# Kernel optimization log

Measured on AMD Instinct MI355X. Metric: run time of the kernel, lower is better.

The kernel has to match this reference:

```python
import jax, jax.numpy as jnp
import numpy as np


def setup_inputs() -> dict:
    key = jax.random.key(0)
    ks = jax.random.split(key, 8)
    B, D, H, W = 4, 96, 64, 64
    K, N, R = 4, 16, 6
    return {
        "x": jax.random.normal(ks[0], (B, D, H, W), jnp.float32),
        "x_proj_weight": jax.random.normal(ks[1], (K, R + 2 * N, D), jnp.float32) * 0.05,
        "dt_projs_weight": jax.random.normal(ks[2], (K, D, R), jnp.float32) * 0.1,
        "dt_projs_bias": jax.random.normal(ks[3], (K, D), jnp.float32) * 0.1,
        "A_logs": jax.random.uniform(ks[4], (K * D, N), jnp.float32),
        "Ds": jax.random.normal(ks[5], (K * D,), jnp.float32),
        "ln_weight": jnp.ones((D,), jnp.float32),
        "ln_bias": jnp.zeros((D,), jnp.float32),
    }


def reference(x, x_proj_weight, dt_projs_weight, dt_projs_bias, A_logs, Ds, ln_weight, ln_bias):
    B, D, H, W = x.shape
    K, _, R = dt_projs_weight.shape
    N = A_logs.shape[1]
    L = H * W

    # ---- CrossScan: 4 traversal orders (row-major, col-major, and their reverses) ----
    xf = x.reshape(B, D, L)                                   # row-major
    xt = jnp.transpose(x, (0, 1, 3, 2)).reshape(B, D, L)      # col-major
    xs = jnp.stack([xf, xt, xf[..., ::-1], xt[..., ::-1]], axis=1)  # (B, K, D, L)

    # ---- input-dependent projections ----
    x_dbl = jnp.einsum('bkdl,kcd->bkcl', xs, x_proj_weight)   # (B, K, R+2N, L)
    dts, Bs, Cs = jnp.split(x_dbl, [R, R + N], axis=2)        # Bs/Cs: (B, K, N, L)
    dts = jnp.einsum('bkrl,kdr->bkdl', dts, dt_projs_weight)  # (B, K, D, L)

    A = -jnp.exp(A_logs).reshape(K, D, N)                     # (K, D, N)
    delta = jax.nn.softplus(dts + dt_projs_bias[None, :, :, None])  # (B, K, D, L)

    # ---- selective (S6) scan over L ----
    def step(h, inp):
        d_t, u_t, B_t, C_t = inp  # (B,K,D) (B,K,D) (B,K,N) (B,K,N)
        dA = jnp.exp(d_t[..., None] * A[None])                # (B,K,D,N)
        h = h * dA + (d_t * u_t)[..., None] * B_t[:, :, None, :]
        y_t = jnp.einsum('bkdn,bkn->bkd', h, C_t)
        return h, y_t

    h0 = jnp.zeros((B, K, D, N), x.dtype)
    seq = (jnp.moveaxis(delta, -1, 0), jnp.moveaxis(xs, -1, 0),
           jnp.moveaxis(Bs, -1, 0), jnp.moveaxis(Cs, -1, 0))
    _, ys = jax.lax.scan(step, h0, seq)                       # (L, B, K, D)
    ys = jnp.moveaxis(ys, 0, -1)                              # (B, K, D, L)
    ys = ys + Ds.reshape(K, D)[None, :, :, None] * xs         # skip term D*u

    # ---- CrossMerge: undo the 4 traversal orders and sum ----
    m = ys[:, 0:2] + ys[:, 2:4][..., ::-1]                    # (B, 2, D, L)
    y = m[:, 0] + jnp.transpose(m[:, 1].reshape(B, D, W, H), (0, 1, 3, 2)).reshape(B, D, L)

    # ---- out_norm (LayerNorm over channels, v0 path) ----
    y = jnp.transpose(y, (0, 2, 1))                           # (B, L, D)
    mu = y.mean(-1, keepdims=True)
    var = y.var(-1, keepdims=True)
    y = (y - mu) / jnp.sqrt(var + 1e-5) * ln_weight + ln_bias
    return y.reshape(B, H, W, D)
```

## Files before the change

kernel.cpp:

```cpp
#include <hip/hip_runtime.h>
#include <math.h>

#define B_ 4
#define D_ 96
#define H_ 64
#define W_ 64
#define L_ 4096
#define K_ 4
#define N_ 16
#define R_ 6
#define C_ 38
#define SSX 128
#define CLSX (L_ / SSX)
#define CH_ (B_ * K_ * D_ * N_)

#if defined(__has_builtin)
#if __has_builtin(__builtin_amdgcn_exp2f)
#define EXP2F(x) __builtin_amdgcn_exp2f(x)
#else
#define EXP2F(x) exp2f(x)
#endif
#else
#define EXP2F(x) exp2f(x)
#endif
#define LOG2E 1.44269504f

__device__ __forceinline__ int src_idx(int k, int l) {
    int m = (k >= 2) ? (L_ - 1 - l) : l;
    if (k & 1) return ((m & 63) << 6) | (m >> 6);
    return m;
}

__device__ __forceinline__ float softplus_f(float a) {
    return (a > 15.f) ? a : __logf(1.f + __expf(a));
}

__global__ __launch_bounds__(256) void transpose_kernel(
    const float* __restrict__ x,
    float* __restrict__ xs2)
{
    int bid = blockIdx.x;
    int b = bid / (3 * 64);
    int rest = bid % (3 * 64);
    int dblk = rest / 64, lblk = rest % 64;
    int d0 = dblk * 32;
    int l0 = lblk * 64;
    int tid = threadIdx.x;

    __shared__ float s_t[32][65];

    for (int i = tid; i < 32 * 64; i += 256) {
        int d = i >> 6, l = i & 63;
        s_t[d][l] = x[((long)b * D_ + d0 + d) * L_ + l0 + l];
    }
    __syncthreads();

    for (int i = tid; i < 64 * 32; i += 256) {
        int l = i >> 5, d = i & 31;
        float v = s_t[d][l];
        xs2[((long)b * L_ + l0 + l) * D_ + d0 + d] = v;
        xs2[((long)(B_ + b) * L_ + l * 64 + lblk) * D_ + d0 + d] = v;
    }
}

__global__ __launch_bounds__(256) void proj_scan_kernel(
    const float* __restrict__ xs2,
    const float* __restrict__ xpw,
    const float* __restrict__ wdt,
    const float* __restrict__ bdt,
    const float* __restrict__ A_logs,
    float* __restrict__ delta,
    float* __restrict__ Bsb,
    float* __restrict__ Csb,
    float* __restrict__ pAarr,
    float* __restrict__ hharr)
{
    const int TL = 64;
    const int tiles = L_ / TL;
    int bid = blockIdx.x;
    int bk = bid / tiles;
    int tile = bid % tiles;
    int b = bk / K_, k = bk % K_;
    int l0 = tile * TL;
    int tid = threadIdx.x;

    __shared__ __align__(16) float s_wpT[D_ * 40];
    __shared__ __align__(16) float s_xs[D_ * 68];
    __shared__ __align__(16) float s_wdt[R_ * D_];
    __shared__ __align__(16) float s_bias[D_];
    __shared__ __align__(16) float s_dts[R_ * 68];
    __shared__ __align__(16) float s_B[TL * N_];

    for (int i = tid; i < C_ * D_; i += 256) {
        int d = i / C_, c = i % C_;
        int cp = (c < 6) ? c : c + 2;
        s_wpT[d * 40 + cp] = xpw[(k * C_ + c) * D_ + d];
    }
    for (int i = tid; i < 96; i += 256) {
        s_wpT[i * 40 + 6] = 0.f;
        s_wpT[i * 40 + 7] = 0.f;
    }
    for (int i = tid; i < R_ * D_; i += 256) {
        int r = i / D_, d = i % D_;
        s_wdt[i] = wdt[(k * D_ + d) * R_ + r];
    }
    if (tid < D_) s_bias[tid] = bdt[k * D_ + tid];

    const float* xsp = xs2 + (long)((k & 1) * B_ + b) * L_ * D_;
    for (int i = tid; i < TL * 24; i += 256) {
        int lt = i / 24, dq = i % 24;
        int row = (k < 2) ? (l0 + lt) : (L_ - 1 - l0 - lt);
        float4 v = *(const float4*)(xsp + (long)row * D_ + dq * 4);
        s_xs[(dq * 4 + 0) * 68 + lt] = v.x;
        s_xs[(dq * 4 + 1) * 68 + lt] = v.y;
        s_xs[(dq * 4 + 2) * 68 + lt] = v.z;
        s_xs[(dq * 4 + 3) * 68 + lt] = v.w;
    }
    __syncthreads();

    long base = (long)bk * L_ + l0;

    int ct = tid >> 4;
    int lt4 = (tid & 15) * 4;
    if (ct < 10) {
        int cp0 = ct * 4;
        float acc[4][4];
#pragma unroll
        for (int i = 0; i < 4; ++i)
#pragma unroll
            for (int j = 0; j < 4; ++j) acc[i][j] = 0.f;
#pragma unroll 4
        for (int d = 0; d < D_; ++d) {
            float4 wv = *(const float4*)(&s_wpT[d * 40 + cp0]);
            float4 xv = *(const float4*)(&s_xs[d * 68 + lt4]);
            float wa[4] = {wv.x, wv.y, wv.z, wv.w};
            float xa[4] = {xv.x, xv.y, xv.z, xv.w};
#pragma unroll
            for (int ci = 0; ci < 4; ++ci)
#pragma unroll
                for (int li = 0; li < 4; ++li)
                    acc[ci][li] += wa[ci] * xa[li];
        }
        if (ct == 0) {
#pragma unroll
            for (int ci = 0; ci < 4; ++ci)
                *(float4*)(&s_dts[ci * 68 + lt4]) =
                    make_float4(acc[ci][0], acc[ci][1], acc[ci][2], acc[ci][3]);
        } else if (ct == 1) {
#pragma unroll
            for (int ci = 0; ci < 2; ++ci)
                *(float4*)(&s_dts[(4 + ci) * 68 + lt4]) =
                    make_float4(acc[ci][0], acc[ci][1], acc[ci][2], acc[ci][3]);
        } else if (ct < 6) {
            int n0 = cp0 - 8;
#pragma unroll
            for (int li = 0; li < 4; ++li) {
                float4 v = make_float4(acc[0][li], acc[1][li], acc[2][li], acc[3][li]);
                *(float4*)(&Bsb[(base + lt4 + li) * N_ + n0]) = v;
                *(float4*)(&s_B[(lt4 + li) * N_ + n0]) = v;
            }
        } else {
            int n0 = cp0 - 24;
#pragma unroll
            for (int li = 0; li < 4; ++li)
                *(float4*)(&Csb[(base + lt4 + li) * N_ + n0]) =
                    make_float4(acc[0][li], acc[1][li], acc[2][li], acc[3][li]);
        }
    }
    __syncthreads();

    for (int tt = tid; tt < 24 * 16; tt += 256) {
        int dt = tt % 24, lt4b = (tt / 24) * 4;
        int d0 = dt * 4;
        float4 bias = *(const float4*)(&s_bias[d0]);
        float acc[4][4];
#pragma unroll
        for (int li = 0; li < 4; ++li) {
            acc[li][0] = bias.x; acc[li][1] = bias.y;
            acc[li][2] = bias.z; acc[li][3] = bias.w;
        }
#pragma unroll
        for (int r = 0; r < R_; ++r) {
            float4 wv = *(const float4*)(&s_wdt[r * D_ + d0]);
            float4 tv = *(const float4*)(&s_dts[r * 68 + lt4b]);
            float wa[4] = {wv.x, wv.y, wv.z, wv.w};
            float ta[4] = {tv.x, tv.y, tv.z, tv.w};
#pragma unroll
            for (int li = 0; li < 4; ++li)
#pragma unroll
                for (int di = 0; di < 4; ++di)
                    acc[li][di] += ta[li] * wa[di];
        }
#pragma unroll
        for (int li = 0; li < 4; ++li) {
            float4 o = make_float4(softplus_f(acc[li][0]), softplus_f(acc[li][1]),
                                   softplus_f(acc[li][2]), softplus_f(acc[li][3]));
            *(float4*)(&delta[(base + lt4b + li) * D_ + d0]) = o;
        }
    }

    if (tid < 192) {
        int sub = tid / 96;
        int dd = tid % 96;
        int j = tile * 2 + sub;
        int kd = k * D_ + dd;

        float A2[16];
        {
            const float4* ap = (const float4*)(A_logs + kd * N_);
#pragma unroll
            for (int q = 0; q < 4; ++q) {
                float4 a = ap[q];
                A2[q * 4 + 0] = -__expf(a.x) * LOG2E;
                A2[q * 4 + 1] = -__expf(a.y) * LOG2E;
                A2[q * 4 + 2] = -__expf(a.z) * LOG2E;
                A2[q * 4 + 3] = -__expf(a.w) * LOG2E;
            }
        }
        float wdtr[R_];
#pragma unroll
        for (int r = 0; r < R_; ++r) wdtr[r] = s_wdt[r * D_ + dd];
        float biasv = s_bias[dd];

        float h[16];
#pragma unroll
        for (int i = 0; i < 16; ++i) h[i] = 0.f;
        float sdel = 0.f;

#pragma unroll 4
        for (int t = 0; t < CLSX; ++t) {
            int lt = sub * CLSX + t;
            float acc = biasv;
#pragma unroll
            for (int r = 0; r < R_; ++r) acc += wdtr[r] * s_dts[r * 68 + lt];
            float del = softplus_f(acc);
            float u = s_xs[dd * 68 + lt];
            float Bv[16];
            *(float4*)(Bv + 0)  = *(const float4*)(&s_B[lt * N_ + 0]);
            *(float4*)(Bv + 4)  = *(const float4*)(&s_B[lt * N_ + 4]);
            *(float4*)(Bv + 8)  = *(const float4*)(&s_B[lt * N_ + 8]);
            *(float4*)(Bv + 12) = *(const float4*)(&s_B[lt * N_ + 12]);
            sdel += del;
            float delu = del * u;
#pragma unroll
            for (int i = 0; i < 16; ++i) {
                float dA = EXP2F(del * A2[i]);
                h[i] = h[i] * dA + delu * Bv[i];
            }
        }

        long sbase = (long)j * CH_ + (long)(bk * D_ + dd) * N_;
#pragma unroll
        for (int q = 0; q < 4; ++q) {
            *(float4*)(pAarr + sbase + q * 4) =
                make_float4(EXP2F(A2[q * 4 + 0] * sdel), EXP2F(A2[q * 4 + 1] * sdel),
                            EXP2F(A2[q * 4 + 2] * sdel), EXP2F(A2[q * 4 + 3] * sdel));
            *(float4*)(hharr + sbase + q * 4) =
                make_float4(h[q * 4], h[q * 4 + 1], h[q * 4 + 2], h[q * 4 + 3]);
        }
    }
}

__global__ __launch_bounds__(256) void scan_combine(
    const float* __restrict__ pAarr,
    float* __restrict__ hharr)
{
    int c = blockIdx.x * 256 + threadIdx.x;
    float h = 0.f;
#pragma unroll 8
    for (int j = 0; j < SSX; ++j) {
        long idx = (long)j * CH_ + c;
        float tmp = hharr[idx];
        float pa  = pAarr[idx];
        hharr[idx] = h;
        h = tmp + pa * h;
    }
}

__global__ __launch_bounds__(384) void scan_part2_pair(
    const float* __restrict__ A_logs,
    const float* __restrict__ Ds,
    const float* __restrict__ xs2,
    const float* __restrict__ delta,
    const float* __restrict__ Bsb,
    const float* __restrict__ Csb,
    const float* __restrict__ hharr,
    float* __restrict__ ypair)
{
    __shared__ float s_y[2][CLSX][D_];

    int bid = blockIdx.x;
    int b = bid / (2 * SSX);
    int rest = bid % (2 * SSX);
    int p = rest / SSX;
    int j = rest % SSX;
    int tid = threadIdx.x;
    int g = tid / 192;
    int r = tid % 192;
    int dd = r >> 1;
    int half = r & 1;
    int n0 = half * 8;

    int kdir = p + 2 * g;
    int bk = b * K_ + kdir;
    int jj = g ? (SSX - 1 - j) : j;
    int l0s = jj * CLSX;
    int kd = kdir * D_ + dd;

    float A2[8];
    {
        const float4* ap = (const float4*)(A_logs + kd * N_ + n0);
        float4 a0 = ap[0], a1 = ap[1];
        A2[0] = -__expf(a0.x) * LOG2E; A2[1] = -__expf(a0.y) * LOG2E;
        A2[2] = -__expf(a0.z) * LOG2E; A2[3] = -__expf(a0.w) * LOG2E;
        A2[4] = -__expf(a1.x) * LOG2E; A2[5] = -__expf(a1.y) * LOG2E;
        A2[6] = -__expf(a1.z) * LOG2E; A2[7] = -__expf(a1.w) * LOG2E;
    }
    float Dv = Ds[kd];

    const float* dp = delta + ((long)bk * L_ + l0s) * D_ + dd;
    const float* bp = Bsb + ((long)bk * L_ + l0s) * N_ + n0;
    const float* cp = Csb + ((long)bk * L_ + l0s) * N_ + n0;
    const float* xsp = xs2 + (long)(p * B_ + b) * L_ * D_;
    long urow0 = g ? ((long)j * CLSX + CLSX - 1) : (long)l0s;
    long ustep = g ? -D_ : D_;
    const float* up = xsp + urow0 * D_ + dd;

    float h[8];
    {
        long sbase = (long)jj * CH_ + (long)(bk * D_ + dd) * N_ + n0;
        float4 h0 = *(const float4*)(hharr + sbase);
        float4 h1 = *(const float4*)(hharr + sbase + 4);
        h[0] = h0.x; h[1] = h0.y; h[2] = h0.z; h[3] = h0.w;
        h[4] = h1.x; h[5] = h1.y; h[6] = h1.z; h[7] = h1.w;
    }

#pragma unroll 4
    for (int t = 0; t < CLSX; ++t) {
        float del = dp[(long)t * D_];
        float u   = up[(long)t * ustep];
        float4 b0 = *(const float4*)(bp + t * N_);
        float4 b1 = *(const float4*)(bp + t * N_ + 4);
        float4 c0 = *(const float4*)(cp + t * N_);
        float4 c1 = *(const float4*)(cp + t * N_ + 4);
        float Bv[8] = {b0.x, b0.y, b0.z, b0.w, b1.x, b1.y, b1.z, b1.w};
        float Cv[8] = {c0.x, c0.y, c0.z, c0.w, c1.x, c1.y, c1.z, c1.w};
        float delu = del * u;
        float yv = 0.f;
#pragma unroll
        for (int i = 0; i < 8; ++i) {
            float dA = EXP2F(del * A2[i]);
            h[i] = h[i] * dA + delu * Bv[i];
            yv += h[i] * Cv[i];
        }
        yv += __shfl_xor(yv, 1);
        if (half == 0) {
            int tpos = g ? (CLSX - 1 - t) : t;
            s_y[g][tpos][dd] = yv + Dv * u;
        }
    }
    __syncthreads();

    float* yo = ypair + ((long)(p * B_ + b) * L_ + (long)j * CLSX) * D_;
    for (int i = tid; i < CLSX * 24; i += 384) {
        int lt = i / 24, dq = i % 24;
        int d0 = dq * 4;
        float4 o = make_float4(s_y[0][lt][d0 + 0] + s_y[1][lt][d0 + 0],
                               s_y[0][lt][d0 + 1] + s_y[1][lt][d0 + 1],
                               s_y[0][lt][d0 + 2] + s_y[1][lt][d0 + 2],
                               s_y[0][lt][d0 + 3] + s_y[1][lt][d0 + 3]);
        *(float4*)(yo + (long)lt * D_ + d0) = o;
    }
}

__global__ __launch_bounds__(256) void ln_merge_kernel(
    const float* __restrict__ ypair,
    const float* __restrict__ lnw,
    const float* __restrict__ lnb,
    float* __restrict__ out)
{
    int wid = (blockIdx.x * 256 + threadIdx.x) >> 6;
    int lane = threadIdx.x & 63;
    int b = wid / L_;
    int m = wid % L_;
    int mt = ((m & 63) << 6) | (m >> 6);

    const float* y0 = ypair + ((long)b * L_ + m) * D_;
    const float* y1 = ypair + ((long)(B_ + b) * L_ + mt) * D_;

    float v0 = y0[lane] + y1[lane];
    float v1 = (lane < 32) ? (y0[64 + lane] + y1[64 + lane]) : 0.f;

    float s  = v0 + v1;
    float s2 = v0 * v0 + v1 * v1;
#pragma unroll
    for (int mm = 1; mm < 64; mm <<= 1) {
        s  += __shfl_xor(s, mm);
        s2 += __shfl_xor(s2, mm);
    }
    float mu  = s * (1.f / D_);
    float var = s2 * (1.f / D_) - mu * mu;
    float rstd = rsqrtf(var + 1e-5f);

    long obase = (long)wid * D_;
    out[obase + lane] = (v0 - mu) * rstd * lnw[lane] + lnb[lane];
    if (lane < 32)
        out[obase + 64 + lane] = (v1 - mu) * rstd * lnw[64 + lane] + lnb[64 + lane];
}

__global__ __launch_bounds__(256) void proj_legacy(
    const float* __restrict__ x,
    const float* __restrict__ xpw,
    const float* __restrict__ wdt,
    const float* __restrict__ bdt,
    float* __restrict__ delta,
    float* __restrict__ Bsb,
    float* __restrict__ Csb)
{
    const int TL = 64;
    const int tiles = L_ / TL;
    int bid = blockIdx.x;
    int bk = bid / tiles;
    int tile = bid % tiles;
    int b = bk / K_, k = bk % K_;
    int l0 = tile * TL;
    int tid = threadIdx.x;

    __shared__ float s_wp[C_ * D_];
    __shared__ float s_wdt[R_ * D_];
    __shared__ float s_bias[D_];
    __shared__ float s_xs[D_ * (TL + 1)];
    __shared__ float s_xdbl[C_ * (TL + 1)];

    for (int i = tid; i < C_ * D_; i += 256) s_wp[i] = xpw[k * C_ * D_ + i];
    for (int i = tid; i < R_ * D_; i += 256) {
        int r = i / D_, d = i % D_;
        s_wdt[i] = wdt[(k * D_ + d) * R_ + r];
    }
    if (tid < D_) s_bias[tid] = bdt[k * D_ + tid];
    for (int i = tid; i < D_ * TL; i += 256) {
        int d = i / TL, lt = i % TL;
        s_xs[d * (TL + 1) + lt] = x[(b * D_ + d) * L_ + src_idx(k, l0 + lt)];
    }
    __syncthreads();

    for (int idx = tid; idx < C_ * TL; idx += 256) {
        int c = idx / TL, lt = idx % TL;
        const float* wr = &s_wp[c * D_];
        float acc = 0.f;
#pragma unroll 8
        for (int d = 0; d < D_; ++d) acc += wr[d] * s_xs[d * (TL + 1) + lt];
        s_xdbl[c * (TL + 1) + lt] = acc;
    }
    __syncthreads();

    long base = (long)bk * L_ + l0;
    for (int idx = tid; idx < TL * D_; idx += 256) {
        int lt = idx / D_, d = idx % D_;
        float acc = s_bias[d];
#pragma unroll
        for (int r = 0; r < R_; ++r)
            acc += s_wdt[r * D_ + d] * s_xdbl[r * (TL + 1) + lt];
        delta[(base + lt) * D_ + d] = softplus_f(acc);
    }
    for (int idx = tid; idx < TL * 2 * N_; idx += 256) {
        int lt = idx / (2 * N_), c2 = idx % (2 * N_);
        float v = s_xdbl[(R_ + c2) * (TL + 1) + lt];
        if (c2 < N_) Bsb[(base + lt) * N_ + c2] = v;
        else         Csb[(base + lt) * N_ + (c2 - N_)] = v;
    }
}

__global__ __launch_bounds__(64) void scan_serial(
    const float* __restrict__ x,
    const float* __restrict__ A_logs,
    const float* __restrict__ Ds,
    const float* __restrict__ delta,
    const float* __restrict__ Bsb,
    const float* __restrict__ Csb,
    float* __restrict__ ys)
{
    const int chans = D_ / 4;
    int bid = blockIdx.x;
    int bk = bid / chans;
    int d0 = (bid % chans) * 4;
    int b = bk / K_, k = bk % K_;
    int lane = threadIdx.x;
    int g = lane >> 4, n = lane & 15;
    int d = d0 + g;
    int kd = k * D_ + d;

    float A  = -__expf(A_logs[kd * N_ + n]);
    float Dv = Ds[kd];
    const float* dptr = delta + ((long)bk * L_) * D_ + d;
    const float* bptr = Bsb + (long)bk * L_ * N_ + n;
    const float* cptr = Csb + (long)bk * L_ * N_ + n;
    const float* xptr = x + ((long)b * D_ + d) * L_;
    float* yptr = ys + ((long)bk * L_) * D_ + d;

    float h = 0.f;
#pragma unroll 4
    for (int l = 0; l < L_; ++l) {
        float del = dptr[(long)l * D_];
        float u   = xptr[src_idx(k, l)];
        float Bt  = bptr[l * N_];
        float Ct  = cptr[l * N_];
        float dA  = __expf(del * A);
        h = h * dA + del * u * Bt;
        float yv = h * Ct;
        yv += __shfl_xor(yv, 1);
        yv += __shfl_xor(yv, 2);
        yv += __shfl_xor(yv, 4);
        yv += __shfl_xor(yv, 8);
        if (n == 0) yptr[(long)l * D_] = yv + Dv * u;
    }
}

__global__ __launch_bounds__(256) void merge_ln_kernel(
    const float* __restrict__ ys,
    const float* __restrict__ lnw,
    const float* __restrict__ lnb,
    float* __restrict__ out)
{
    int wid = (blockIdx.x * 256 + threadIdx.x) >> 6;
    int lane = threadIdx.x & 63;
    int b = wid / L_;
    int l = wid % L_;
    int lt = ((l & 63) << 6) | (l >> 6);

    long base0 = ((long)(b * K_ + 0) * L_ + l) * D_;
    long base2 = ((long)(b * K_ + 2) * L_ + (L_ - 1 - l)) * D_;
    long base1 = ((long)(b * K_ + 1) * L_ + lt) * D_;
    long base3 = ((long)(b * K_ + 3) * L_ + (L_ - 1 - lt)) * D_;

    int dA = lane;
    int dB = lane + 64;
    float v0 = ys[base0 + dA] + ys[base2 + dA] + ys[base1 + dA] + ys[base3 + dA];
    float v1 = 0.f;
    if (dB < D_)
        v1 = ys[base0 + dB] + ys[base2 + dB] + ys[base1 + dB] + ys[base3 + dB];

    float s  = v0 + v1;
    float s2 = v0 * v0 + v1 * v1;
#pragma unroll
    for (int m = 1; m < 64; m <<= 1) {
        s  += __shfl_xor(s, m);
        s2 += __shfl_xor(s2, m);
    }
    float mu  = s * (1.f / D_);
    float var = s2 * (1.f / D_) - mu * mu;
    float rstd = rsqrtf(var + 1e-5f);

    long obase = ((long)b * L_ + l) * D_;
    out[obase + dA] = (v0 - mu) * rstd * lnw[dA] + lnb[dA];
    if (dB < D_)
        out[obase + dB] = (v1 - mu) * rstd * lnw[dB] + lnb[dB];
}

extern "C" void kernel_launch(void* const* d_in, const int* in_sizes, int n_in,
                              void* d_out, int out_size, void* d_ws, size_t ws_size,
                              hipStream_t stream) {
    const float* x      = (const float*)d_in[0];
    const float* xpw    = (const float*)d_in[1];
    const float* wdt    = (const float*)d_in[2];
    const float* bdt    = (const float*)d_in[3];
    const float* A_logs = (const float*)d_in[4];
    const float* Ds     = (const float*)d_in[5];
    const float* lnw    = (const float*)d_in[6];
    const float* lnb    = (const float*)d_in[7];
    float* out = (float*)d_out;

    float* ws = (float*)d_ws;
    const long n_delta = (long)B_ * K_ * L_ * D_;
    const long n_bc    = (long)B_ * K_ * L_ * N_;
    const long n_bld   = (long)B_ * L_ * D_;
    const long n_sum   = (long)SSX * CH_;

    float* delta = ws;
    float* Bsb   = delta + n_delta;
    float* Csb   = Bsb + n_bc;
    float* xs2   = Csb + n_bc;
    float* ypair = xs2 + 2 * n_bld;
    float* hharr = ypair + 2 * n_bld;
    float* pAarr = ypair;
    size_t need = (size_t)(n_delta + 2 * n_bc + 4 * n_bld + n_sum) * 4;

    if (ws_size >= need) {
        transpose_kernel<<<B_ * 3 * 64, 256, 0, stream>>>(x, xs2);
        proj_scan_kernel<<<B_ * K_ * (L_ / 64), 256, 0, stream>>>(
            xs2, xpw, wdt, bdt, A_logs, delta, Bsb, Csb, pAarr, hharr);
        scan_combine<<<CH_ / 256, 256, 0, stream>>>(pAarr, hharr);
        scan_part2_pair<<<B_ * 2 * SSX, 384, 0, stream>>>(
            A_logs, Ds, xs2, delta, Bsb, Csb, hharr, ypair);
        ln_merge_kernel<<<(B_ * L_) / 4, 256, 0, stream>>>(ypair, lnw, lnb, out);
    } else {
        float* ys2 = Csb + n_bc;
        proj_legacy<<<B_ * K_ * (L_ / 64), 256, 0, stream>>>(
            x, xpw, wdt, bdt, delta, Bsb, Csb);
        scan_serial<<<B_ * K_ * (D_ / 4), 64, 0, stream>>>(
            x, A_logs, Ds, delta, Bsb, Csb, ys2);
        merge_ln_kernel<<<(B_ * L_) / 4, 256, 0, stream>>>(ys2, lnw, lnb, out);
    }
}
```

Baseline: 182.6 us.

## Store low-rank dt projections instead of full delta, recompute delta in scan pass

Instead of writing the full softplus(delta) tensor (B*K*L*D floats) to global memory, the projection kernel now stores only the 6 rank-R dt values per position, padded to 8. The second scan pass recomputes delta from these values with a 6-term dot product and a softplus per step. This cuts a large global write and read in exchange for extra per-step arithmetic and transcendental work. The chunk scan in the projection kernel also reads u from global xs2 instead of shared memory, and the combine loop unroll is raised.

```diff
diff --git a/kernel.cpp b/kernel.cpp
--- a/kernel.cpp
+++ b/kernel.cpp
@@ -69,7 +69,7 @@
     const float* __restrict__ wdt,
     const float* __restrict__ bdt,
     const float* __restrict__ A_logs,
-    float* __restrict__ delta,
+    float* __restrict__ dts_g,
     float* __restrict__ Bsb,
     float* __restrict__ Csb,
     float* __restrict__ pAarr,
@@ -169,34 +169,15 @@
     }
     __syncthreads();
 
-    for (int tt = tid; tt < 24 * 16; tt += 256) {
-        int dt = tt % 24, lt4b = (tt / 24) * 4;
-        int d0 = dt * 4;
-        float4 bias = *(const float4*)(&s_bias[d0]);
-        float acc[4][4];
-#pragma unroll
-        for (int li = 0; li < 4; ++li) {
-            acc[li][0] = bias.x; acc[li][1] = bias.y;
-            acc[li][2] = bias.z; acc[li][3] = bias.w;
-        }
-#pragma unroll
-        for (int r = 0; r < R_; ++r) {
-            float4 wv = *(const float4*)(&s_wdt[r * D_ + d0]);
-            float4 tv = *(const float4*)(&s_dts[r * 68 + lt4b]);
-            float wa[4] = {wv.x, wv.y, wv.z, wv.w};
-            float ta[4] = {tv.x, tv.y, tv.z, tv.w};
-#pragma unroll
-            for (int li = 0; li < 4; ++li)
-#pragma unroll
-                for (int di = 0; di < 4; ++di)
-                    acc[li][di] += ta[li] * wa[di];
-        }
-#pragma unroll
-        for (int li = 0; li < 4; ++li) {
-            float4 o = make_float4(softplus_f(acc[li][0]), softplus_f(acc[li][1]),
-                                   softplus_f(acc[li][2]), softplus_f(acc[li][3]));
-            *(float4*)(&delta[(base + lt4b + li) * D_ + d0]) = o;
-        }
+    for (int i = tid; i < TL * 2; i += 256) {
+        int lt = i >> 1, q = i & 1;
+        float4 v;
+        if (q == 0)
+            v = make_float4(s_dts[0 * 68 + lt], s_dts[1 * 68 + lt],
+                            s_dts[2 * 68 + lt], s_dts[3 * 68 + lt]);
+        else
+            v = make_float4(s_dts[4 * 68 + lt], s_dts[5 * 68 + lt], 0.f, 0.f);
+        *(float4*)(&dts_g[(base + lt) * 8 + q * 4]) = v;
     }
 
     if (tid < 192) {
@@ -222,6 +203,11 @@
         for (int r = 0; r < R_; ++r) wdtr[r] = s_wdt[r * D_ + dd];
         float biasv = s_bias[dd];
 
+        int lts0 = sub * CLSX;
+        long urow0 = (k < 2) ? (long)(l0 + lts0) : (long)(L_ - 1 - l0 - lts0);
+        long ustep = (k < 2) ? D_ : -D_;
+        const float* up = xsp + urow0 * D_ + dd;
+
         float h[16];
 #pragma unroll
         for (int i = 0; i < 16; ++i) h[i] = 0.f;
@@ -229,12 +215,12 @@
 
 #pragma unroll 4
         for (int t = 0; t < CLSX; ++t) {
-            int lt = sub * CLSX + t;
+            int lt = lts0 + t;
             float acc = biasv;
 #pragma unroll
             for (int r = 0; r < R_; ++r) acc += wdtr[r] * s_dts[r * 68 + lt];
             float del = softplus_f(acc);
-            float u = s_xs[dd * 68 + lt];
+            float u = up[(long)t * ustep];
             float Bv[16];
             *(float4*)(Bv + 0)  = *(const float4*)(&s_B[lt * N_ + 0]);
             *(float4*)(Bv + 4)  = *(const float4*)(&s_B[lt * N_ + 4]);
@@ -267,7 +253,7 @@
 {
     int c = blockIdx.x * 256 + threadIdx.x;
     float h = 0.f;
-#pragma unroll 8
+#pragma unroll 16
     for (int j = 0; j < SSX; ++j) {
         long idx = (long)j * CH_ + c;
         float tmp = hharr[idx];
@@ -280,8 +266,10 @@
 __global__ __launch_bounds__(384) void scan_part2_pair(
     const float* __restrict__ A_logs,
     const float* __restrict__ Ds,
+    const float* __restrict__ wdt,
+    const float* __restrict__ bdt,
     const float* __restrict__ xs2,
-    const float* __restrict__ delta,
+    const float* __restrict__ dts_g,
     const float* __restrict__ Bsb,
     const float* __restrict__ Csb,
     const float* __restrict__ hharr,
@@ -317,8 +305,12 @@
         A2[6] = -__expf(a1.z) * LOG2E; A2[7] = -__expf(a1.w) * LOG2E;
     }
     float Dv = Ds[kd];
-
-    const float* dp = delta + ((long)bk * L_ + l0s) * D_ + dd;
+    float wdtr[R_];
+#pragma unroll
+    for (int rr = 0; rr < R_; ++rr) wdtr[rr] = wdt[kd * R_ + rr];
+    float biasv = bdt[kd];
+
+    const float* tp = dts_g + ((long)bk * L_ + l0s) * 8;
     const float* bp = Bsb + ((long)bk * L_ + l0s) * N_ + n0;
     const float* cp = Csb + ((long)bk * L_ + l0s) * N_ + n0;
     const float* xsp = xs2 + (long)(p * B_ + b) * L_ * D_;
@@ -337,7 +329,16 @@
 
 #pragma unroll 4
     for (int t = 0; t < CLSX; ++t) {
-        float del = dp[(long)t * D_];
+        float4 t0 = *(const float4*)(tp + t * 8);
+        float4 t1 = *(const float4*)(tp + t * 8 + 4);
+        float acc = biasv;
+        acc += wdtr[0] * t0.x;
+        acc += wdtr[1] * t0.y;
+        acc += wdtr[2] * t0.z;
+        acc += wdtr[3] * t0.w;
+        acc += wdtr[4] * t1.x;
+        acc += wdtr[5] * t1.y;
+        float del = softplus_f(acc);
         float u   = up[(long)t * ustep];
         float4 b0 = *(const float4*)(bp + t * N_);
         float4 b1 = *(const float4*)(bp + t * N_ + 4);
@@ -571,34 +572,38 @@
     float* out = (float*)d_out;
 
     float* ws = (float*)d_ws;
-    const long n_delta = (long)B_ * K_ * L_ * D_;
+    const long n_dts   = (long)B_ * K_ * L_ * 8;
     const long n_bc    = (long)B_ * K_ * L_ * N_;
     const long n_bld   = (long)B_ * L_ * D_;
     const long n_sum   = (long)SSX * CH_;
 
-    float* delta = ws;
-    float* Bsb   = delta + n_delta;
+    float* dts_g = ws;
+    float* Bsb   = dts_g + n_dts;
     float* Csb   = Bsb + n_bc;
     float* xs2   = Csb + n_bc;
     float* ypair = xs2 + 2 * n_bld;
     float* hharr = ypair + 2 * n_bld;
     float* pAarr = ypair;
-    size_t need = (size_t)(n_delta + 2 * n_bc + 4 * n_bld + n_sum) * 4;
+    size_t need = (size_t)(n_dts + 2 * n_bc + 4 * n_bld + n_sum) * 4;
 
     if (ws_size >= need) {
         transpose_kernel<<<B_ * 3 * 64, 256, 0, stream>>>(x, xs2);
         proj_scan_kernel<<<B_ * K_ * (L_ / 64), 256, 0, stream>>>(
-            xs2, xpw, wdt, bdt, A_logs, delta, Bsb, Csb, pAarr, hharr);
+            xs2, xpw, wdt, bdt, A_logs, dts_g, Bsb, Csb, pAarr, hharr);
         scan_combine<<<CH_ / 256, 256, 0, stream>>>(pAarr, hharr);
         scan_part2_pair<<<B_ * 2 * SSX, 384, 0, stream>>>(
-            A_logs, Ds, xs2, delta, Bsb, Csb, hharr, ypair);
+            A_logs, Ds, wdt, bdt, xs2, dts_g, Bsb, Csb, hharr, ypair);
         ln_merge_kernel<<<(B_ * L_) / 4, 256, 0, stream>>>(ypair, lnw, lnb, out);
     } else {
-        float* ys2 = Csb + n_bc;
+        const long n_delta = (long)B_ * K_ * L_ * D_;
+        float* delta = ws;
+        float* Bsb2  = delta + n_delta;
+        float* Csb2  = Bsb2 + n_bc;
+        float* ys2   = Csb2 + n_bc;
         proj_legacy<<<B_ * K_ * (L_ / 64), 256, 0, stream>>>(
-            x, xpw, wdt, bdt, delta, Bsb, Csb);
+            x, xpw, wdt, bdt, delta, Bsb2, Csb2);
         scan_serial<<<B_ * K_ * (D_ / 4), 64, 0, stream>>>(
-            x, A_logs, Ds, delta, Bsb, Csb, ys2);
+            x, A_logs, Ds, delta, Bsb2, Csb2, ys2);
         merge_ln_kernel<<<(B_ * L_) / 4, 256, 0, stream>>>(ys2, lnw, lnb, out);
     }
 }
```

After: 199.8 us. 1.09x slower.
